# Kernel tuning notes

Measured on AMD Instinct MI355X. Metric: run time of the kernel, lower is better.

## Reference

```python
import jax, jax.numpy as jnp
import numpy as np

N_NODES = 200000
MAX_DEG = 128
S1, S2 = 25, 10  # neighbor sample sizes per hop (GraphSAGE defaults)


def setup_inputs() -> dict:
    key = jax.random.key(0)
    ks = jax.random.split(key, 9)
    F, H, C, B = 256, 128, 41, 1024
    return {
        "node_ids": jax.random.randint(ks[0], (B,), 0, N_NODES, dtype=jnp.int32),
        "features": jax.random.normal(ks[1], (N_NODES, F), dtype=jnp.float32),
        "adj_info": jax.random.randint(ks[2], (N_NODES, MAX_DEG), 0, N_NODES, dtype=jnp.int32),
        "W_self1": jax.random.normal(ks[3], (F, H), dtype=jnp.float32) * 0.05,
        "W_neigh1": jax.random.normal(ks[4], (F, H), dtype=jnp.float32) * 0.05,
        "W_self2": jax.random.normal(ks[5], (2 * H, H), dtype=jnp.float32) * 0.05,
        "W_neigh2": jax.random.normal(ks[6], (2 * H, H), dtype=jnp.float32) * 0.05,
        "W_pred": jax.random.normal(ks[7], (2 * H, C), dtype=jnp.float32) * 0.05,
        "b_pred": jnp.zeros((C,), dtype=jnp.float32),
    }


def _sample(adj_info, node_ids):
    """Uniform neighbor sampling: hop1 [B,S1], hop2 [B,S1,S2]."""
    k1, k2 = jax.random.split(jax.random.key(42))
    B = node_ids.shape[0]
    cols1 = jax.random.randint(k1, (B, S1), 0, MAX_DEG)
    hop1 = jnp.take_along_axis(adj_info[node_ids], cols1, axis=1)  # [B,S1]
    cols2 = jax.random.randint(k2, (B * S1, S2), 0, MAX_DEG)
    hop2 = jnp.take_along_axis(adj_info[hop1.reshape(-1)], cols2, axis=1)
    return hop1, hop2.reshape(B, S1, S2)


def _mean_agg(self_f, neigh_f, Ws, Wn, act):
    # GraphSAGE MeanAggregator with concat: [self@Ws ; mean(neigh)@Wn]
    neigh = neigh_f.mean(axis=-2)
    return act(jnp.concatenate([self_f @ Ws, neigh @ Wn], axis=-1))


def reference(node_ids, features, adj_info, W_self1, W_neigh1, W_self2, W_neigh2, W_pred, b_pred):
    hop1, hop2 = _sample(adj_info, node_ids)
    f0 = features[node_ids]      # [B,F]
    f1 = features[hop1]          # [B,S1,F]
    f2 = features[hop2]          # [B,S1,S2,F]

    h0 = _mean_agg(f0, f1, W_self1, W_neigh1, jax.nn.relu)   # [B,2H]
    h1 = _mean_agg(f1, f2, W_self1, W_neigh1, jax.nn.relu)   # [B,S1,2H]
    h = _mean_agg(h0, h1, W_self2, W_neigh2, lambda x: x)    # [B,2H]

    # tf.math.l2_normalize(x, 1): x * rsqrt(max(sum(x^2), 1e-12))
    h = h * jax.lax.rsqrt(jnp.maximum(jnp.sum(h * h, axis=1, keepdims=True), 1e-12))
    logits = h @ W_pred + b_pred
    return jax.nn.softmax(logits, axis=-1)
```

## Files before the change

kernel.cpp:

```cpp
#include <hip/hip_runtime.h>
#include <cstdint>
#include <cstddef>

#define BATCH 1024
#define S1 25
#define S2 10
#define FDIM 256
#define HDIM 128
#define NCLS 41
#define MAXDEG 128

typedef __attribute__((ext_vector_type(8))) short bf16x8;
typedef __attribute__((ext_vector_type(4))) float f32x4;

__host__ __device__ static inline void tf2x32(uint32_t k0, uint32_t k1,
                                              uint32_t c0, uint32_t c1,
                                              uint32_t& o0, uint32_t& o1) {
  const uint32_t ks2 = k0 ^ k1 ^ 0x1BD11BDAu;
  uint32_t x0 = c0 + k0, x1 = c1 + k1;
#define TFR(r) { x0 += x1; x1 = (x1 << (r)) | (x1 >> (32 - (r))); x1 ^= x0; }
  TFR(13) TFR(15) TFR(26) TFR(6)
  x0 += k1;  x1 += ks2 + 1u;
  TFR(17) TFR(29) TFR(16) TFR(24)
  x0 += ks2; x1 += k0 + 2u;
  TFR(13) TFR(15) TFR(26) TFR(6)
  x0 += k0;  x1 += k1 + 3u;
  TFR(17) TFR(29) TFR(16) TFR(24)
  x0 += k1;  x1 += ks2 + 4u;
  TFR(13) TFR(15) TFR(26) TFR(6)
  x0 += ks2; x1 += k0 + 5u;
#undef TFR
  o0 = x0; o1 = x1;
}

__device__ static inline uint32_t rand_bits_at(uint32_t kb0, uint32_t kb1, uint32_t j) {
  uint32_t o0, o1;
  tf2x32(kb0, kb1, 0u, j, o0, o1);
  return o0 ^ o1;
}

__device__ static inline ushort f2bf(float x) {
  uint32_t u = __float_as_uint(x);
  return (ushort)((u + 0x7fffu + ((u >> 16) & 1u)) >> 16);
}

__global__ __launch_bounds__(256)
void wprep_kernel(const float* __restrict__ Ws1, const float* __restrict__ Wn1,
                  ushort* __restrict__ WbT) {
  const int idx = blockIdx.x;
  const int h = idx >> 7, n = idx & 127;
  const float* W = h ? Wn1 : Ws1;
  WbT[(size_t)idx * FDIM + threadIdx.x] = f2bf(W[(size_t)threadIdx.x * HDIM + n]);
}

__device__ static inline void mfma_half(const ushort (*As)[32][40],
                                        const ushort* __restrict__ Bmat,
                                        float* __restrict__ dst,
                                        int wave, int lq, int lr) {
  f32x4 acc[2][2];
#pragma unroll
  for (int rt = 0; rt < 2; ++rt)
#pragma unroll
    for (int ct = 0; ct < 2; ++ct) acc[rt][ct] = (f32x4)(0.f);

#pragma unroll
  for (int k0 = 0; k0 < 8; ++k0) {
    bf16x8 b0 = *(const bf16x8*)(Bmat + (size_t)(wave * 32 + lr) * FDIM + k0 * 32 + lq * 8);
    bf16x8 b1 = *(const bf16x8*)(Bmat + (size_t)(wave * 32 + 16 + lr) * FDIM + k0 * 32 + lq * 8);
    bf16x8 a0 = *(const bf16x8*)&As[k0][lr][lq * 8];
    bf16x8 a1 = *(const bf16x8*)&As[k0][16 + lr][lq * 8];
    acc[0][0] = __builtin_amdgcn_mfma_f32_16x16x32_bf16(a0, b0, acc[0][0], 0, 0, 0);
    acc[0][1] = __builtin_amdgcn_mfma_f32_16x16x32_bf16(a0, b1, acc[0][1], 0, 0, 0);
    acc[1][0] = __builtin_amdgcn_mfma_f32_16x16x32_bf16(a1, b0, acc[1][0], 0, 0, 0);
    acc[1][1] = __builtin_amdgcn_mfma_f32_16x16x32_bf16(a1, b1, acc[1][1], 0, 0, 0);
  }

#pragma unroll
  for (int ct = 0; ct < 2; ++ct) {
    float s = 0.f;
#pragma unroll
    for (int rt = 0; rt < 2; ++rt)
#pragma unroll
      for (int r = 0; r < 4; ++r)
        s += fmaxf(acc[rt][ct][r], 0.f);
    s += __shfl_xor(s, 16, 64);
    s += __shfl_xor(s, 32, 64);
    if (lq == 0) dst[wave * 32 + ct * 16 + lr] = s * (1.f / S1);
  }
}

__global__ __launch_bounds__(256, 4)
void mega_kernel(const int* __restrict__ node_ids, const float* __restrict__ feat,
                 const int* __restrict__ adj, const ushort* __restrict__ WbT,
                 const float* __restrict__ Ws1, const float* __restrict__ Wn1,
                 const float* __restrict__ Ws2, const float* __restrict__ Wn2,
                 const float* __restrict__ Wp, const float* __restrict__ bp,
                 float* __restrict__ out,
                 uint32_t kb1_0, uint32_t kb1_1, uint32_t kb2_0, uint32_t kb2_1) {
  const int b = blockIdx.x;
  const int t = threadIdx.x;
  const int wave = t >> 6, lane = t & 63;
  const int lq = lane >> 4, lr = lane & 15;

  __shared__ int    hop1s[S1];
  __shared__ int    hop2s[S1 * S2];
  __shared__ ushort As[8][32][40];
  __shared__ float  F0[FDIM];
  __shared__ float  N1[4][FDIM];
  __shared__ float  H1M[2 * HDIM];
  __shared__ float  H0[2 * HDIM];
  __shared__ float  HN[2 * HDIM];
  __shared__ float  red[4];
  __shared__ float  lg[NCLS];
  __shared__ float  smx[2];

  const int nid = node_ids[b];

  if (t < S1 * S2) {
    const int s1 = t / S2;
    uint32_t c1 = rand_bits_at(kb1_0, kb1_1, (uint32_t)(b * S1 + s1)) & (MAXDEG - 1);
    const int h1 = adj[(size_t)nid * MAXDEG + c1];
    if (t == s1 * S2) hop1s[s1] = h1;
    uint32_t c2 = rand_bits_at(kb2_0, kb2_1, (uint32_t)(b * S1 * S2 + t)) & (MAXDEG - 1);
    hop2s[t] = adj[(size_t)h1 * MAXDEG + c2];
  }
  if (t < 64) ((float4*)F0)[t] = ((const float4*)(feat + (size_t)nid * FDIM))[t];
  {
    ushort4 z; z.x = 0; z.y = 0; z.z = 0; z.w = 0;
    for (int i = t; i < 448; i += 256) {
      const int rc = i >> 3, q = i & 7;
      const int r = 25 + (rc >> 3), ch = rc & 7;
      *(ushort4*)&As[ch][r][q * 4] = z;
    }
  }
  __syncthreads();

  ushort4 nm[7];
  {
    float ax = 0.f, ay = 0.f, az = 0.f, aw = 0.f;
#pragma unroll
    for (int i = 0; i < 7; ++i) {
      const int s1 = wave + i * 4;
      if (s1 < S1) {
        const int rid1 = hop1s[s1];
        float4 v = ((const float4*)(feat + (size_t)rid1 * FDIM))[lane];
        float bx = 0.f, by = 0.f, bz = 0.f, bw = 0.f;
#pragma unroll
        for (int r = 0; r < S2; ++r) {
          const int rid = hop2s[s1 * S2 + r];
          float4 w = ((const float4*)(feat + (size_t)rid * FDIM))[lane];
          bx += w.x; by += w.y; bz += w.z; bw += w.w;
        }
        ax += v.x; ay += v.y; az += v.z; aw += v.w;
        ushort4 o1;
        o1.x = f2bf(v.x); o1.y = f2bf(v.y); o1.z = f2bf(v.z); o1.w = f2bf(v.w);
        *(ushort4*)&As[lane >> 3][s1][(lane & 7) * 4] = o1;
        const float inv2 = 1.f / S2;
        ushort4 o2;
        o2.x = f2bf(bx * inv2); o2.y = f2bf(by * inv2);
        o2.z = f2bf(bz * inv2); o2.w = f2bf(bw * inv2);
        nm[i] = o2;
      }
    }
    float4 p; p.x = ax; p.y = ay; p.z = az; p.w = aw;
    ((float4*)N1[wave])[lane] = p;
  }
  __syncthreads();

  mfma_half(As, WbT, H1M, wave, lq, lr);
  __syncthreads();

#pragma unroll
  for (int i = 0; i < 7; ++i) {
    const int s1 = wave + i * 4;
    if (s1 < S1) *(ushort4*)&As[lane >> 3][s1][(lane & 7) * 4] = nm[i];
  }
  {
    const float s = N1[0][t] + N1[1][t] + N1[2][t] + N1[3][t];
    N1[0][t] = s * (1.f / S1);
  }
  __syncthreads();

  mfma_half(As, WbT + (size_t)HDIM * FDIM, H1M + HDIM, wave, lq, lr);
  __syncthreads();

  const int hh = t >> 7, c = t & 127;
  {
    const float* W = hh ? Wn1 : Ws1;
    const float* Ap = hh ? N1[0] : F0;
    float acc = 0.f;
#pragma unroll 8
    for (int k4 = 0; k4 < 64; ++k4) {
      float4 a = ((const float4*)Ap)[k4];
      acc += a.x * W[(size_t)(k4 * 4 + 0) * HDIM + c]
           + a.y * W[(size_t)(k4 * 4 + 1) * HDIM + c]
           + a.z * W[(size_t)(k4 * 4 + 2) * HDIM + c]
           + a.w * W[(size_t)(k4 * 4 + 3) * HDIM + c];
    }
    H0[t] = fmaxf(acc, 0.f);
  }
  __syncthreads();

  float hv;
  {
    const float* W = hh ? Wn2 : Ws2;
    const float* Ap = hh ? H1M : H0;
    float acc = 0.f;
#pragma unroll 8
    for (int k4 = 0; k4 < 64; ++k4) {
      float4 a = ((const float4*)Ap)[k4];
      acc += a.x * W[(size_t)(k4 * 4 + 0) * HDIM + c]
           + a.y * W[(size_t)(k4 * 4 + 1) * HDIM + c]
           + a.z * W[(size_t)(k4 * 4 + 2) * HDIM + c]
           + a.w * W[(size_t)(k4 * 4 + 3) * HDIM + c];
    }
    hv = acc;
  }

  {
    float s = hv * hv;
#pragma unroll
    for (int off = 32; off; off >>= 1) s += __shfl_xor(s, off, 64);
    if (lane == 0) red[wave] = s;
  }
  __syncthreads();
  {
    const float scl = rsqrtf(fmaxf(red[0] + red[1] + red[2] + red[3], 1e-12f));
    HN[t] = hv * scl;
  }
  __syncthreads();

  {
    const int g = t >> 2, q = t & 3;
    if (g < NCLS) {
      float s = 0.f;
#pragma unroll 8
      for (int k = 0; k < 64; ++k)
        s += HN[q * 64 + k] * Wp[(size_t)(q * 64 + k) * NCLS + g];
      s += __shfl_xor(s, 1, 64);
      s += __shfl_xor(s, 2, 64);
      if (q == 0) lg[g] = s + bp[g];
    }
  }
  __syncthreads();
  if (t == 0) {
    float m = -1e30f;
    for (int i = 0; i < NCLS; ++i) m = fmaxf(m, lg[i]);
    float ssum = 0.f;
    for (int i = 0; i < NCLS; ++i) ssum += expf(lg[i] - m);
    smx[0] = m; smx[1] = ssum;
  }
  __syncthreads();
  if (t < NCLS)
    out[(size_t)b * NCLS + t] = expf(lg[t] - smx[0]) / smx[1];
}

extern "C" void kernel_launch(void* const* d_in, const int* in_sizes, int n_in,
                              void* d_out, int out_size, void* d_ws, size_t ws_size,
                              hipStream_t stream) {
  const int*   node_ids = (const int*)d_in[0];
  const float* features = (const float*)d_in[1];
  const int*   adj      = (const int*)d_in[2];
  const float* Ws1      = (const float*)d_in[3];
  const float* Wn1      = (const float*)d_in[4];
  const float* Ws2      = (const float*)d_in[5];
  const float* Wn2      = (const float*)d_in[6];
  const float* Wp       = (const float*)d_in[7];
  const float* bp       = (const float*)d_in[8];
  float* out = (float*)d_out;

  ushort* WbT = (ushort*)d_ws;

  uint32_t k1_0, k1_1, k2_0, k2_1, kb1_0, kb1_1, kb2_0, kb2_1;
  tf2x32(0u, 42u, 0u, 0u, k1_0, k1_1);
  tf2x32(0u, 42u, 0u, 1u, k2_0, k2_1);
  tf2x32(k1_0, k1_1, 0u, 1u, kb1_0, kb1_1);
  tf2x32(k2_0, k2_1, 0u, 1u, kb2_0, kb2_1);

  wprep_kernel<<<256, 256, 0, stream>>>(Ws1, Wn1, WbT);

  mega_kernel<<<BATCH, 256, 0, stream>>>(node_ids, features, adj, WbT,
                                         Ws1, Wn1, Ws2, Wn2, Wp, bp, out,
                                         kb1_0, kb1_1, kb2_0, kb2_1);
}
```

Before: 388.1 us.

## Fold root-node layer-1 matmul into MFMA padding row and defer hop-2 gathers

The root node's features and its neighbor mean now go into the spare row 25 of the bf16 MFMA A tile, so the scalar fp32 layer-1 GEMV for h0 is dropped and its result is read from the MFMA accumulators. The hop-1 feature loads are batched into registers up front, and the hop-2 gather is moved to after the first MFMA so its registers are not held across it. This removes a full pass over Ws1/Wn1 per block and lowers register pressure. In exchange, h0 is now computed in bf16 instead of fp32, which can reduce accuracy.

```diff
diff --git a/kernel.cpp b/kernel.cpp
--- a/kernel.cpp
+++ b/kernel.cpp
@@ -55,7 +55,8 @@
 
 __device__ static inline void mfma_half(const ushort (*As)[32][40],
                                         const ushort* __restrict__ Bmat,
-                                        float* __restrict__ dst,
+                                        float* __restrict__ dstMean,
+                                        float* __restrict__ dstH0,
                                         int wave, int lq, int lr) {
   f32x4 acc[2][2];
 #pragma unroll
@@ -77,22 +78,26 @@
 
 #pragma unroll
   for (int ct = 0; ct < 2; ++ct) {
+    const int n = wave * 32 + ct * 16 + lr;
+    if (lq == 2) dstH0[n] = fmaxf(acc[1][ct][1], 0.f);
     float s = 0.f;
 #pragma unroll
     for (int rt = 0; rt < 2; ++rt)
 #pragma unroll
-      for (int r = 0; r < 4; ++r)
-        s += fmaxf(acc[rt][ct][r], 0.f);
+      for (int r = 0; r < 4; ++r) {
+        float val = fmaxf(acc[rt][ct][r], 0.f);
+        if (rt == 1 && r == 1) val = (lq == 2) ? 0.f : val;
+        s += val;
+      }
     s += __shfl_xor(s, 16, 64);
     s += __shfl_xor(s, 32, 64);
-    if (lq == 0) dst[wave * 32 + ct * 16 + lr] = s * (1.f / S1);
+    if (lq == 0) dstMean[n] = s * (1.f / S1);
   }
 }
 
 __global__ __launch_bounds__(256, 4)
 void mega_kernel(const int* __restrict__ node_ids, const float* __restrict__ feat,
                  const int* __restrict__ adj, const ushort* __restrict__ WbT,
-                 const float* __restrict__ Ws1, const float* __restrict__ Wn1,
                  const float* __restrict__ Ws2, const float* __restrict__ Wn2,
                  const float* __restrict__ Wp, const float* __restrict__ bp,
                  float* __restrict__ out,
@@ -105,7 +110,6 @@
   __shared__ int    hop1s[S1];
   __shared__ int    hop2s[S1 * S2];
   __shared__ ushort As[8][32][40];
-  __shared__ float  F0[FDIM];
   __shared__ float  N1[4][FDIM];
   __shared__ float  H1M[2 * HDIM];
   __shared__ float  H0[2 * HDIM];
@@ -124,42 +128,38 @@
     uint32_t c2 = rand_bits_at(kb2_0, kb2_1, (uint32_t)(b * S1 * S2 + t)) & (MAXDEG - 1);
     hop2s[t] = adj[(size_t)h1 * MAXDEG + c2];
   }
-  if (t < 64) ((float4*)F0)[t] = ((const float4*)(feat + (size_t)nid * FDIM))[t];
+  if (t < 64) {
+    float4 v = ((const float4*)(feat + (size_t)nid * FDIM))[t];
+    ushort4 o;
+    o.x = f2bf(v.x); o.y = f2bf(v.y); o.z = f2bf(v.z); o.w = f2bf(v.w);
+    *(ushort4*)&As[t >> 3][25][(t & 7) * 4] = o;
+  }
   {
     ushort4 z; z.x = 0; z.y = 0; z.z = 0; z.w = 0;
-    for (int i = t; i < 448; i += 256) {
+    for (int i = t; i < 384; i += 256) {
       const int rc = i >> 3, q = i & 7;
-      const int r = 25 + (rc >> 3), ch = rc & 7;
+      const int r = 26 + (rc >> 3), ch = rc & 7;
       *(ushort4*)&As[ch][r][q * 4] = z;
     }
   }
   __syncthreads();
 
-  ushort4 nm[7];
-  {
+  {
+    float4 v[7];
+#pragma unroll
+    for (int i = 0; i < 7; ++i) {
+      const int s1 = wave + i * 4;
+      if (s1 < S1) v[i] = ((const float4*)(feat + (size_t)hop1s[s1] * FDIM))[lane];
+    }
     float ax = 0.f, ay = 0.f, az = 0.f, aw = 0.f;
 #pragma unroll
     for (int i = 0; i < 7; ++i) {
       const int s1 = wave + i * 4;
       if (s1 < S1) {
-        const int rid1 = hop1s[s1];
-        float4 v = ((const float4*)(feat + (size_t)rid1 * FDIM))[lane];
-        float bx = 0.f, by = 0.f, bz = 0.f, bw = 0.f;
-#pragma unroll
-        for (int r = 0; r < S2; ++r) {
-          const int rid = hop2s[s1 * S2 + r];
-          float4 w = ((const float4*)(feat + (size_t)rid * FDIM))[lane];
-          bx += w.x; by += w.y; bz += w.z; bw += w.w;
-        }
-        ax += v.x; ay += v.y; az += v.z; aw += v.w;
-        ushort4 o1;
-        o1.x = f2bf(v.x); o1.y = f2bf(v.y); o1.z = f2bf(v.z); o1.w = f2bf(v.w);
-        *(ushort4*)&As[lane >> 3][s1][(lane & 7) * 4] = o1;
-        const float inv2 = 1.f / S2;
-        ushort4 o2;
-        o2.x = f2bf(bx * inv2); o2.y = f2bf(by * inv2);
-        o2.z = f2bf(bz * inv2); o2.w = f2bf(bw * inv2);
-        nm[i] = o2;
+        ax += v[i].x; ay += v[i].y; az += v[i].z; aw += v[i].w;
+        ushort4 o;
+        o.x = f2bf(v[i].x); o.y = f2bf(v[i].y); o.z = f2bf(v[i].z); o.w = f2bf(v[i].w);
+        *(ushort4*)&As[lane >> 3][s1][(lane & 7) * 4] = o;
       }
     }
     float4 p; p.x = ax; p.y = ay; p.z = az; p.w = aw;
@@ -167,40 +167,36 @@
   }
   __syncthreads();
 
-  mfma_half(As, WbT, H1M, wave, lq, lr);
-  __syncthreads();
-
-#pragma unroll
+  mfma_half(As, WbT, H1M, H0, wave, lq, lr);
+  __syncthreads();
+
+  {
+    const float nv = (N1[0][t] + N1[1][t] + N1[2][t] + N1[3][t]) * (1.f / S1);
+    As[t >> 5][25][t & 31] = f2bf(nv);
+  }
   for (int i = 0; i < 7; ++i) {
     const int s1 = wave + i * 4;
-    if (s1 < S1) *(ushort4*)&As[lane >> 3][s1][(lane & 7) * 4] = nm[i];
-  }
-  {
-    const float s = N1[0][t] + N1[1][t] + N1[2][t] + N1[3][t];
-    N1[0][t] = s * (1.f / S1);
-  }
-  __syncthreads();
-
-  mfma_half(As, WbT + (size_t)HDIM * FDIM, H1M + HDIM, wave, lq, lr);
+    if (s1 < S1) {
+      float bx = 0.f, by = 0.f, bz = 0.f, bw = 0.f;
+#pragma unroll
+      for (int r = 0; r < S2; ++r) {
+        const int rid = hop2s[s1 * S2 + r];
+        float4 w = ((const float4*)(feat + (size_t)rid * FDIM))[lane];
+        bx += w.x; by += w.y; bz += w.z; bw += w.w;
+      }
+      const float inv2 = 1.f / S2;
+      ushort4 o;
+      o.x = f2bf(bx * inv2); o.y = f2bf(by * inv2);
+      o.z = f2bf(bz * inv2); o.w = f2bf(bw * inv2);
+      *(ushort4*)&As[lane >> 3][s1][(lane & 7) * 4] = o;
+    }
+  }
+  __syncthreads();
+
+  mfma_half(As, WbT + (size_t)HDIM * FDIM, H1M + HDIM, H0 + HDIM, wave, lq, lr);
   __syncthreads();
 
   const int hh = t >> 7, c = t & 127;
-  {
-    const float* W = hh ? Wn1 : Ws1;
-    const float* Ap = hh ? N1[0] : F0;
-    float acc = 0.f;
-#pragma unroll 8
-    for (int k4 = 0; k4 < 64; ++k4) {
-      float4 a = ((const float4*)Ap)[k4];
-      acc += a.x * W[(size_t)(k4 * 4 + 0) * HDIM + c]
-           + a.y * W[(size_t)(k4 * 4 + 1) * HDIM + c]
-           + a.z * W[(size_t)(k4 * 4 + 2) * HDIM + c]
-           + a.w * W[(size_t)(k4 * 4 + 3) * HDIM + c];
-    }
-    H0[t] = fmaxf(acc, 0.f);
-  }
-  __syncthreads();
-
   float hv;
   {
     const float* W = hh ? Wn2 : Ws2;
@@ -280,6 +276,6 @@
   wprep_kernel<<<256, 256, 0, stream>>>(Ws1, Wn1, WbT);
 
   mega_kernel<<<BATCH, 256, 0, stream>>>(node_ids, features, adj, WbT,
-                                         Ws1, Wn1, Ws2, Wn2, Wp, bp, out,
+                                         Ws2, Wn2, Wp, bp, out,
                                          kb1_0, kb1_1, kb2_0, kb2_1);
 }
```

Result: faster. 358.6 us (-7.6%).
